# Kernel tuning notes

Measured on AMD Instinct MI355X. Metric: run time of the kernel, lower is better.

The kernel has to match this reference:

```python
import jax, jax.numpy as jnp
import numpy as np

N, E, D, H, ED = 50000, 800000, 128, 8, 64
C = D // H  # head dim = 16


def _ln(x, g, b, eps=1e-5):
    m = jnp.mean(x, axis=-1, keepdims=True)
    v = jnp.var(x, axis=-1, keepdims=True)
    return (x - m) * jax.lax.rsqrt(v + eps) * g + b


def setup_inputs() -> dict:
    key = jax.random.key(0)
    ks = jax.random.split(key, 16)
    p = lambda k, shape: (jax.random.normal(k, shape, dtype=jnp.float32) * 0.05)
    return {
        "x": jax.random.normal(ks[0], (N, D), dtype=jnp.float32),
        "edge_index": jax.random.randint(ks[1], (2, E), 0, N, dtype=jnp.int64),
        "edge_attr": jax.random.normal(ks[2], (E, ED), dtype=jnp.float32),
        "Wq": p(ks[3], (D, D)), "bq": jnp.zeros((D,), jnp.float32),
        "Wk": p(ks[4], (D, D)), "bk": jnp.zeros((D,), jnp.float32),
        "Wv": p(ks[5], (D, D)), "bv": jnp.zeros((D,), jnp.float32),
        "We": p(ks[6], (ED, D)),  # lin_edge has no bias in PyG TransformerConv
        "Wskip": p(ks[7], (D, D)), "bskip": jnp.zeros((D,), jnp.float32),
        "g1": jnp.ones((D,), jnp.float32), "b1": jnp.zeros((D,), jnp.float32),
        "g2": jnp.ones((D,), jnp.float32), "b2": jnp.zeros((D,), jnp.float32),
        "Wf1": p(ks[8], (D, 4 * D)), "bf1": jnp.zeros((4 * D,), jnp.float32),
        "Wf2": p(ks[9], (4 * D, D)), "bf2": jnp.zeros((D,), jnp.float32),
    }


def reference(x, edge_index, edge_attr, Wq, bq, Wk, bk, Wv, bv, We,
              Wskip, bskip, g1, b1, g2, b2, Wf1, bf1, Wf2, bf2):
    n = x.shape[0]
    src, dst = edge_index[0], edge_index[1]  # message flows src (j) -> dst (i)
    q = (x @ Wq + bq).reshape(n, H, C)
    k = (x @ Wk + bk).reshape(n, H, C)
    v = (x @ Wv + bv).reshape(n, H, C)
    e = (edge_attr @ We).reshape(-1, H, C)
    k_j = k[src] + e            # [E,H,C]
    v_j = v[src] + e            # [E,H,C]
    logits = jnp.sum(q[dst] * k_j, axis=-1) / np.sqrt(C)  # [E,H]
    # segment softmax over edges grouped by destination node
    m = jax.ops.segment_max(logits, dst, num_segments=n)   # [N,H]
    ex = jnp.exp(logits - m[dst])
    denom = jax.ops.segment_sum(ex, dst, num_segments=n)   # [N,H]
    alpha = ex / denom[dst]                                 # [E,H]
    agg = jax.ops.segment_sum(alpha[..., None] * v_j, dst, num_segments=n)
    conv = agg.reshape(n, D) + x @ Wskip + bskip            # root_weight skip
    h = _ln(conv + x, g1, b1)
    ffn = jax.nn.gelu(h @ Wf1 + bf1, approximate=False) @ Wf2 + bf2
    return _ln(ffn + h, g2, b2)
```

## Files before the change

### kernel.cpp

```cpp
#include <hip/hip_runtime.h>

#define NN 50000
#define NE 800000

__global__ __launch_bounds__(256) void init_int_kernel(int* __restrict__ a, int n) {
  int i = blockIdx.x * 256 + threadIdx.x;
  if (i < n) a[i] = 0;
}

__global__ __launch_bounds__(256) void hist_kernel(const int* __restrict__ ei,
                                                   int* __restrict__ deg) {
  int e = blockIdx.x * 256 + threadIdx.x;
  if (e < NE) {
    int d = ei[NE + e];
    if ((unsigned)d >= NN) d = 0;
    atomicAdd(&deg[d], 1);
  }
}

__global__ __launch_bounds__(1024) void scan_kernel(const int* __restrict__ deg,
                                                    int* __restrict__ offs) {
  __shared__ int part[1024];
  int tid = threadIdx.x;
  const int chunk = (NN + 1023) / 1024;
  int base = tid * chunk;
  int s = 0;
  for (int j = 0; j < chunk; ++j) {
    int idx = base + j;
    if (idx < NN) s += deg[idx];
  }
  part[tid] = s;
  __syncthreads();
  for (int off = 1; off < 1024; off <<= 1) {
    int t = (tid >= off) ? part[tid - off] : 0;
    __syncthreads();
    part[tid] += t;
    __syncthreads();
  }
  int run = (tid > 0) ? part[tid - 1] : 0;
  for (int j = 0; j < chunk; ++j) {
    int idx = base + j;
    if (idx < NN) { offs[idx] = run; run += deg[idx]; }
  }
  if (tid == 1023) offs[NN] = part[1023];
}

__global__ __launch_bounds__(256) void scatter_kernel(const int* __restrict__ ei,
    const int* __restrict__ offs, int* __restrict__ cursor,
    int* __restrict__ csr_eid, int* __restrict__ csr_src) {
  int e = blockIdx.x * 256 + threadIdx.x;
  if (e < NE) {
    int s = ei[e];
    int d = ei[NE + e];
    if ((unsigned)s >= NN) s = 0;
    if ((unsigned)d >= NN) d = 0;
    int pos = atomicAdd(&cursor[d], 1);
    int slot = offs[d] + pos;
    csr_eid[slot] = e;
    csr_src[slot] = s;
  }
}

__global__ __launch_bounds__(256) void node_proj_kernel(
    const float* __restrict__ x,
    const float* __restrict__ Wq, const float* __restrict__ bq,
    const float* __restrict__ Wk, const float* __restrict__ bk,
    const float* __restrict__ Wv, const float* __restrict__ bv,
    const float* __restrict__ Wsk, const float* __restrict__ bsk,
    float* __restrict__ qo, float* __restrict__ ko, float* __restrict__ vo,
    float* __restrict__ so) {
  __shared__ float xs[64 * 128];
  int tid = threadIdx.x;
  int row0 = blockIdx.x * 64;
  int nrows = NN - row0; if (nrows > 64) nrows = 64;
  const float4* xg = (const float4*)(x + (size_t)row0 * 128);
  float4* xs4 = (float4*)xs;
  int nv = nrows * 32;
  for (int i = tid; i < 64 * 32; i += 256)
    if (i < nv) xs4[i] = xg[i];
  __syncthreads();

  int colg = tid & 31;
  int rowg = tid >> 5;
  const float* Wm[4] = {Wq, Wk, Wv, Wsk};
  const float* bm[4] = {bq, bk, bv, bsk};
  float* om[4] = {qo, ko, vo, so};

  for (int m = 0; m < 4; ++m) {
    const float* W = Wm[m];
    float acc[8][4];
    #pragma unroll
    for (int r = 0; r < 8; ++r)
      #pragma unroll
      for (int c = 0; c < 4; ++c) acc[r][c] = 0.f;
    for (int k0 = 0; k0 < 128; k0 += 4) {
      float4 w0 = *(const float4*)(W + (size_t)(k0 + 0) * 128 + colg * 4);
      float4 w1 = *(const float4*)(W + (size_t)(k0 + 1) * 128 + colg * 4);
      float4 w2 = *(const float4*)(W + (size_t)(k0 + 2) * 128 + colg * 4);
      float4 w3 = *(const float4*)(W + (size_t)(k0 + 3) * 128 + colg * 4);
      #pragma unroll
      for (int r = 0; r < 8; ++r) {
        float4 xv = *(const float4*)(&xs[(rowg * 8 + r) * 128 + k0]);
        acc[r][0] += xv.x * w0.x + xv.y * w1.x + xv.z * w2.x + xv.w * w3.x;
        acc[r][1] += xv.x * w0.y + xv.y * w1.y + xv.z * w2.y + xv.w * w3.y;
        acc[r][2] += xv.x * w0.z + xv.y * w1.z + xv.z * w2.z + xv.w * w3.z;
        acc[r][3] += xv.x * w0.w + xv.y * w1.w + xv.z * w2.w + xv.w * w3.w;
      }
    }
    float4 bb = *(const float4*)(bm[m] + colg * 4);
    float* outp = om[m];
    #pragma unroll
    for (int r = 0; r < 8; ++r) {
      int lr = rowg * 8 + r;
      if (lr < nrows) {
        float4 res;
        res.x = acc[r][0] + bb.x;
        res.y = acc[r][1] + bb.y;
        res.z = acc[r][2] + bb.z;
        res.w = acc[r][3] + bb.w;
        if (m == 0) { res.x *= 0.25f; res.y *= 0.25f; res.z *= 0.25f; res.w *= 0.25f; }
        if (m == 3) {
          res.x += xs[lr * 128 + colg * 4 + 0];
          res.y += xs[lr * 128 + colg * 4 + 1];
          res.z += xs[lr * 128 + colg * 4 + 2];
          res.w += xs[lr * 128 + colg * 4 + 3];
        }
        *(float4*)(outp + (size_t)(row0 + lr) * 128 + colg * 4) = res;
      }
    }
  }
}

__global__ __launch_bounds__(256) void qe_kernel(const float* __restrict__ q,
                                                 const float* __restrict__ We,
                                                 float* __restrict__ qe) {
  long idx = (long)blockIdx.x * 256 + threadIdx.x;
  int n = (int)(idx >> 9);
  int r = (int)(idx & 511);
  int h = r >> 6, j = r & 63;
  const float* qp = q + (size_t)n * 128 + h * 16;
  const float* wp = We + (size_t)j * 128 + h * 16;
  float s = 0.f;
  #pragma unroll
  for (int c = 0; c < 16; ++c) s += qp[c] * wp[c];
  qe[idx] = s;
}

__global__ __launch_bounds__(256) void agg_ln1_kernel(
    const float* __restrict__ q, const float* __restrict__ kb,
    const float* __restrict__ vb, const float* __restrict__ qe,
    const float* __restrict__ ea, const float* __restrict__ skipx,
    const float* __restrict__ We,
    const int* __restrict__ offs, const int* __restrict__ csr_eid,
    const int* __restrict__ csr_src,
    const float* __restrict__ g1, const float* __restrict__ b1,
    float* __restrict__ hbuf) {
  __shared__ float ea_s[4][8][68];
  __shared__ float wea_s[4][8][68];
  int tid = threadIdx.x;
  int wave = tid >> 6;
  int lane = tid & 63;
  int node = blockIdx.x * 4 + wave;
  float (*eas)[68] = ea_s[wave];
  float (*weas)[68] = wea_s[wave];

  int g = lane >> 3;
  int hh = lane & 7;

  float q_r[16];
  {
    const float* qp = q + (size_t)node * 128 + hh * 16;
    #pragma unroll
    for (int u = 0; u < 4; ++u) {
      float4 t = *(const float4*)(qp + 4 * u);
      q_r[4*u+0] = t.x; q_r[4*u+1] = t.y; q_r[4*u+2] = t.z; q_r[4*u+3] = t.w;
    }
  }
  float qe_r[64];
  {
    const float* qp = qe + (size_t)node * 512 + hh * 64;
    #pragma unroll
    for (int u = 0; u < 16; ++u) {
      float4 t = *(const float4*)(qp + 4 * u);
      qe_r[4*u+0] = t.x; qe_r[4*u+1] = t.y; qe_r[4*u+2] = t.z; qe_r[4*u+3] = t.w;
    }
  }
  float wea_r[8];
  #pragma unroll
  for (int j = 0; j < 8; ++j) wea_r[j] = 0.f;
  float wv0 = 0.f, wv1 = 0.f, pden = 0.f;

  int base = offs[node];
  int deg = offs[node + 1] - base;

  for (int t0 = 0; t0 < deg; t0 += 8) {
    int myi = t0 + g;
    int valid = myi < deg;
    int slot = base + (valid ? myi : 0);
    int eid = csr_eid[slot];
    int src = csr_src[slot];

    const float4* eap = (const float4*)(ea + (size_t)eid * 64);
    float4 a0 = eap[hh * 2];
    float4 a1 = eap[hh * 2 + 1];
    *(float4*)(&eas[g][hh * 8]) = a0;
    *(float4*)(&eas[g][hh * 8 + 4]) = a1;
    asm volatile("s_waitcnt lgkmcnt(0)" ::: "memory");

    const float* kp = kb + (size_t)src * 128 + hh * 16;
    float lg = 0.f;
    #pragma unroll
    for (int u = 0; u < 4; ++u) {
      float4 kv = *(const float4*)(kp + 4 * u);
      lg += q_r[4*u+0]*kv.x + q_r[4*u+1]*kv.y + q_r[4*u+2]*kv.z + q_r[4*u+3]*kv.w;
    }
    #pragma unroll
    for (int u = 0; u < 16; ++u) {
      float4 av = *(const float4*)(&eas[g][4 * u]);
      lg += qe_r[4*u+0]*av.x + qe_r[4*u+1]*av.y + qe_r[4*u+2]*av.z + qe_r[4*u+3]*av.w;
    }
    float w = valid ? __expf(lg) : 0.f;
    pden += w;

    #pragma unroll
    for (int g2 = 0; g2 < 8; ++g2) {
      int   sg  = __shfl(src, g2 * 8, 64);
      float wgh = __shfl(w, g2 * 8 + g, 64);
      float2 vv = *(const float2*)(vb + (size_t)sg * 128 + lane * 2);
      wv0 += wgh * vv.x;
      wv1 += wgh * vv.y;
      float4 e0 = *(const float4*)(&eas[g2][hh * 8]);
      float4 e1 = *(const float4*)(&eas[g2][hh * 8 + 4]);
      wea_r[0] += wgh * e0.x; wea_r[1] += wgh * e0.y;
      wea_r[2] += wgh * e0.z; wea_r[3] += wgh * e0.w;
      wea_r[4] += wgh * e1.x; wea_r[5] += wgh * e1.y;
      wea_r[6] += wgh * e1.z; wea_r[7] += wgh * e1.w;
    }
    asm volatile("s_waitcnt lgkmcnt(0)" ::: "memory");
  }

  float den = pden;
  den += __shfl_xor(den, 8, 64);
  den += __shfl_xor(den, 16, 64);
  den += __shfl_xor(den, 32, 64);
  float denf = __shfl(den, g, 64);

  *(float4*)(&weas[g][hh * 8])     = make_float4(wea_r[0], wea_r[1], wea_r[2], wea_r[3]);
  *(float4*)(&weas[g][hh * 8 + 4]) = make_float4(wea_r[4], wea_r[5], wea_r[6], wea_r[7]);
  asm volatile("s_waitcnt lgkmcnt(0)" ::: "memory");

  float s0 = wv0, s1 = wv1;
  const float* wep = We + lane * 2;
  #pragma unroll
  for (int u = 0; u < 16; ++u) {
    float4 ww = *(const float4*)(&weas[g][4 * u]);
    float2 p0 = *(const float2*)(wep + (size_t)(4 * u + 0) * 128);
    float2 p1 = *(const float2*)(wep + (size_t)(4 * u + 1) * 128);
    float2 p2 = *(const float2*)(wep + (size_t)(4 * u + 2) * 128);
    float2 p3 = *(const float2*)(wep + (size_t)(4 * u + 3) * 128);
    s0 += ww.x * p0.x + ww.y * p1.x + ww.z * p2.x + ww.w * p3.x;
    s1 += ww.x * p0.y + ww.y * p1.y + ww.z * p2.y + ww.w * p3.y;
  }
  float inv = (deg > 0) ? 1.f / denf : 0.f;
  float2 skv = *(const float2*)(skipx + (size_t)node * 128 + lane * 2);
  float c0 = s0 * inv + skv.x;
  float c1 = s1 * inv + skv.y;

  float sum = c0 + c1;
  float sq = c0 * c0 + c1 * c1;
  #pragma unroll
  for (int o = 1; o < 64; o <<= 1) {
    sum += __shfl_xor(sum, o, 64);
    sq  += __shfl_xor(sq, o, 64);
  }
  float mean = sum * (1.f / 128.f);
  float var = sq * (1.f / 128.f) - mean * mean;
  float rstd = rsqrtf(var + 1e-5f);
  float2 gg = *(const float2*)(g1 + lane * 2);
  float2 bb = *(const float2*)(b1 + lane * 2);
  float h0 = (c0 - mean) * rstd * gg.x + bb.x;
  float h1 = (c1 - mean) * rstd * gg.y + bb.y;
  *(float2*)(hbuf + (size_t)node * 128 + lane * 2) = make_float2(h0, h1);
}

__global__ __launch_bounds__(256) void ffn_ln2_kernel(
    const float* __restrict__ hbuf,
    const float* __restrict__ Wf1, const float* __restrict__ bf1,
    const float* __restrict__ Wf2, const float* __restrict__ bf2,
    const float* __restrict__ g2v, const float* __restrict__ b2v,
    float* __restrict__ out) {
  __shared__ float hs[16 * 128];
  __shared__ float ts[16][516];
  int tid = threadIdx.x;
  size_t row0 = (size_t)blockIdx.x * 16;
  const float4* hg = (const float4*)(hbuf + row0 * 128);
  float4* hs4 = (float4*)hs;
  hs4[tid] = hg[tid];
  hs4[tid + 256] = hg[tid + 256];
  __syncthreads();

  {
    int colg = tid & 63;
    int rowq = tid >> 6;
    float acc[4][8];
    #pragma unroll
    for (int r = 0; r < 4; ++r)
      #pragma unroll
      for (int c = 0; c < 8; ++c) acc[r][c] = 0.f;
    for (int k0 = 0; k0 < 128; k0 += 4) {
      float hva[4][4];
      #pragma unroll
      for (int r = 0; r < 4; ++r) {
        float4 t = *(const float4*)(&hs[(rowq * 4 + r) * 128 + k0]);
        hva[r][0] = t.x; hva[r][1] = t.y; hva[r][2] = t.z; hva[r][3] = t.w;
      }
      #pragma unroll
      for (int kd = 0; kd < 4; ++kd) {
        float4 w0 = *(const float4*)(Wf1 + (size_t)(k0 + kd) * 512 + colg * 8);
        float4 w1 = *(const float4*)(Wf1 + (size_t)(k0 + kd) * 512 + colg * 8 + 4);
        #pragma unroll
        for (int r = 0; r < 4; ++r) {
          float hv = hva[r][kd];
          acc[r][0] += hv * w0.x; acc[r][1] += hv * w0.y;
          acc[r][2] += hv * w0.z; acc[r][3] += hv * w0.w;
          acc[r][4] += hv * w1.x; acc[r][5] += hv * w1.y;
          acc[r][6] += hv * w1.z; acc[r][7] += hv * w1.w;
        }
      }
    }
    float4 bb0 = *(const float4*)(bf1 + colg * 8);
    float4 bb1 = *(const float4*)(bf1 + colg * 8 + 4);
    float bba[8] = {bb0.x, bb0.y, bb0.z, bb0.w, bb1.x, bb1.y, bb1.z, bb1.w};
    #pragma unroll
    for (int r = 0; r < 4; ++r) {
      #pragma unroll
      for (int c = 0; c < 8; ++c) {
        float val = acc[r][c] + bba[c];
        val = 0.5f * val * (1.f + erff(val * 0.70710678118654752440f));
        ts[rowq * 4 + r][colg * 8 + c] = val;
      }
    }
  }
  __syncthreads();
  {
    int row = tid >> 4;
    int cg = tid & 15;
    float f[8];
    #pragma unroll
    for (int c = 0; c < 8; ++c) f[c] = 0.f;
    for (int k0 = 0; k0 < 512; k0 += 4) {
      float4 tt = *(const float4*)(&ts[row][k0]);
      float tva[4] = {tt.x, tt.y, tt.z, tt.w};
      #pragma unroll
      for (int kd = 0; kd < 4; ++kd) {
        float4 w0 = *(const float4*)(Wf2 + (size_t)(k0 + kd) * 128 + cg * 8);
        float4 w1 = *(const float4*)(Wf2 + (size_t)(k0 + kd) * 128 + cg * 8 + 4);
        float tv = tva[kd];
        f[0] += tv * w0.x; f[1] += tv * w0.y; f[2] += tv * w0.z; f[3] += tv * w0.w;
        f[4] += tv * w1.x; f[5] += tv * w1.y; f[6] += tv * w1.z; f[7] += tv * w1.w;
      }
    }
    float4 bb0 = *(const float4*)(bf2 + cg * 8);
    float4 bb1 = *(const float4*)(bf2 + cg * 8 + 4);
    float4 h0 = *(const float4*)(&hs[row * 128 + cg * 8]);
    float4 h1 = *(const float4*)(&hs[row * 128 + cg * 8 + 4]);
    f[0] += bb0.x + h0.x; f[1] += bb0.y + h0.y; f[2] += bb0.z + h0.z; f[3] += bb0.w + h0.w;
    f[4] += bb1.x + h1.x; f[5] += bb1.y + h1.y; f[6] += bb1.z + h1.z; f[7] += bb1.w + h1.w;

    float sum = 0.f, sq = 0.f;
    #pragma unroll
    for (int c = 0; c < 8; ++c) { sum += f[c]; sq += f[c] * f[c]; }
    #pragma unroll
    for (int o = 1; o < 16; o <<= 1) {
      sum += __shfl_xor(sum, o, 64);
      sq  += __shfl_xor(sq, o, 64);
    }
    float mean = sum * (1.f / 128.f);
    float var = sq * (1.f / 128.f) - mean * mean;
    float rstd = rsqrtf(var + 1e-5f);
    float4 gg0 = *(const float4*)(g2v + cg * 8);
    float4 gg1 = *(const float4*)(g2v + cg * 8 + 4);
    float4 vb0 = *(const float4*)(b2v + cg * 8);
    float4 vb1 = *(const float4*)(b2v + cg * 8 + 4);
    float4 o0, o1;
    o0.x = (f[0] - mean) * rstd * gg0.x + vb0.x;
    o0.y = (f[1] - mean) * rstd * gg0.y + vb0.y;
    o0.z = (f[2] - mean) * rstd * gg0.z + vb0.z;
    o0.w = (f[3] - mean) * rstd * gg0.w + vb0.w;
    o1.x = (f[4] - mean) * rstd * gg1.x + vb1.x;
    o1.y = (f[5] - mean) * rstd * gg1.y + vb1.y;
    o1.z = (f[6] - mean) * rstd * gg1.z + vb1.z;
    o1.w = (f[7] - mean) * rstd * gg1.w + vb1.w;
    float* op = out + (row0 + row) * 128 + cg * 8;
    *(float4*)op = o0;
    *(float4*)(op + 4) = o1;
  }
}

extern "C" void kernel_launch(void* const* d_in, const int* in_sizes, int n_in,
                              void* d_out, int out_size, void* d_ws, size_t ws_size,
                              hipStream_t stream) {
  const float* x   = (const float*)d_in[0];
  const int* ei    = (const int*)d_in[1];
  const float* ea  = (const float*)d_in[2];
  const float* Wq  = (const float*)d_in[3];  const float* bq  = (const float*)d_in[4];
  const float* Wk  = (const float*)d_in[5];  const float* bk  = (const float*)d_in[6];
  const float* Wv  = (const float*)d_in[7];  const float* bv  = (const float*)d_in[8];
  const float* We  = (const float*)d_in[9];
  const float* Wsk = (const float*)d_in[10]; const float* bsk = (const float*)d_in[11];
  const float* g1  = (const float*)d_in[12]; const float* b1  = (const float*)d_in[13];
  const float* g2  = (const float*)d_in[14]; const float* b2  = (const float*)d_in[15];
  const float* Wf1 = (const float*)d_in[16]; const float* bf1 = (const float*)d_in[17];
  const float* Wf2 = (const float*)d_in[18]; const float* bf2 = (const float*)d_in[19];
  float* outp = (float*)d_out;

  char* w = (char*)d_ws;
  float* qb   = (float*)w; w += (size_t)NN * 128 * 4;
  float* kb   = (float*)w; w += (size_t)NN * 128 * 4;
  float* vb   = (float*)w; w += (size_t)NN * 128 * 4;
  float* sk   = (float*)w; w += (size_t)NN * 128 * 4;
  float* hb   = sk;
  float* qeb  = (float*)w; w += (size_t)NN * 512 * 4;
  int* deg    = (int*)w;   w += (size_t)NN * 4;
  int* cursor = (int*)w;   w += (size_t)NN * 4;
  int* offs   = (int*)w;   w += (size_t)(NN + 1) * 4;
  int* ceid   = (int*)w;   w += (size_t)NE * 4;
  int* csrc   = (int*)w;   w += (size_t)NE * 4;

  init_int_kernel<<<(2 * NN + 255) / 256, 256, 0, stream>>>(deg, 2 * NN);
  hist_kernel<<<NE / 256, 256, 0, stream>>>(ei, deg);
  scan_kernel<<<1, 1024, 0, stream>>>(deg, offs);
  scatter_kernel<<<NE / 256, 256, 0, stream>>>(ei, offs, cursor, ceid, csrc);
  node_proj_kernel<<<(NN + 63) / 64, 256, 0, stream>>>(x, Wq, bq, Wk, bk, Wv, bv, Wsk, bsk,
                                                       qb, kb, vb, sk);
  qe_kernel<<<NN * 2, 256, 0, stream>>>(qb, We, qeb);
  agg_ln1_kernel<<<NN / 4, 256, 0, stream>>>(qb, kb, vb, qeb, ea, sk, We,
                                             offs, ceid, csrc, g1, b1, hb);
  ffn_ln2_kernel<<<NN / 16, 256, 0, stream>>>(hb, Wf1, bf1, Wf2, bf2, g2, b2, outp);
}
```

Baseline: 1.723 ms.

## Split fused FFN into LDS-tiled GEMM kernels with split-K partials and LN2 epilogue

Result: slower. 6.836 ms (+296.9%).

```diff
diff --git a/kernel.cpp b/kernel.cpp
--- a/kernel.cpp
+++ b/kernel.cpp
@@ -283,118 +283,136 @@
   *(float2*)(hbuf + (size_t)node * 128 + lane * 2) = make_float2(h0, h1);
 }
 
-__global__ __launch_bounds__(256) void ffn_ln2_kernel(
-    const float* __restrict__ hbuf,
-    const float* __restrict__ Wf1, const float* __restrict__ bf1,
-    const float* __restrict__ Wf2, const float* __restrict__ bf2,
+__device__ __forceinline__ void tile_gemm_body(
+    float* __restrict__ Wlds, float* __restrict__ hls,
+    const float* __restrict__ A, int lda, int kofs,
+    const float* __restrict__ W, int ldw, int kw0, int c0w,
+    const float* __restrict__ bias,
+    bool do_gelu,
+    float* __restrict__ Out, int ldo, int c0o, int row0) {
+  int tid = threadIdx.x;
+  for (int i = tid; i < 128 * 32; i += 256) {
+    int k = i >> 5, cq = i & 31;
+    float4 w = *(const float4*)(W + (size_t)(kw0 + k) * ldw + c0w + cq * 4);
+    Wlds[(cq * 4 + 0) * 132 + k] = w.x;
+    Wlds[(cq * 4 + 1) * 132 + k] = w.y;
+    Wlds[(cq * 4 + 2) * 132 + k] = w.z;
+    Wlds[(cq * 4 + 3) * 132 + k] = w.w;
+  }
+  int c4 = tid & 31;
+  int rp = tid >> 5;
+  float bj[4];
+  #pragma unroll
+  for (int j = 0; j < 4; ++j) bj[j] = bias ? bias[c4 + 32 * j] : 0.f;
+  __syncthreads();
+
+  int rows_blk = NN - row0; if (rows_blk > 256) rows_blk = 256;
+  int nbat = (rows_blk + 15) >> 4;
+  for (int b = 0; b < nbat; ++b) {
+    int rb0 = row0 + b * 16;
+    for (int i = tid; i < 512; i += 256) {
+      int r = i >> 5, qq = i & 31;
+      int gr = rb0 + r;
+      float4 v = make_float4(0.f, 0.f, 0.f, 0.f);
+      if (gr < NN) v = *(const float4*)(A + (size_t)gr * lda + kofs + qq * 4);
+      *(float4*)(hls + r * 128 + qq * 4) = v;
+    }
+    __syncthreads();
+
+    float acc0[4], acc1[4];
+    #pragma unroll
+    for (int j = 0; j < 4; ++j) { acc0[j] = bj[j]; acc1[j] = bj[j]; }
+    int r0 = rp * 2, r1 = rp * 2 + 1;
+    #pragma unroll
+    for (int k0 = 0; k0 < 128; k0 += 4) {
+      float4 h0 = *(const float4*)(hls + r0 * 128 + k0);
+      float4 h1 = *(const float4*)(hls + r1 * 128 + k0);
+      #pragma unroll
+      for (int j = 0; j < 4; ++j) {
+        float4 wv = *(const float4*)(Wlds + (c4 + 32 * j) * 132 + k0);
+        acc0[j] += h0.x * wv.x + h0.y * wv.y + h0.z * wv.z + h0.w * wv.w;
+        acc1[j] += h1.x * wv.x + h1.y * wv.y + h1.z * wv.z + h1.w * wv.w;
+      }
+    }
+
+    int gr0 = rb0 + r0, gr1 = rb0 + r1;
+    #pragma unroll
+    for (int j = 0; j < 4; ++j) {
+      float v0 = acc0[j], v1 = acc1[j];
+      if (do_gelu) {
+        v0 = 0.5f * v0 * (1.f + erff(v0 * 0.70710678118654752440f));
+        v1 = 0.5f * v1 * (1.f + erff(v1 * 0.70710678118654752440f));
+      }
+      int col = c0o + c4 + 32 * j;
+      if (gr0 < NN) Out[(size_t)gr0 * ldo + col] = v0;
+      if (gr1 < NN) Out[(size_t)gr1 * ldo + col] = v1;
+    }
+    __syncthreads();
+  }
+}
+
+__global__ __launch_bounds__(256) void ffn1_kernel(
+    const float* __restrict__ hbuf, const float* __restrict__ Wf1,
+    const float* __restrict__ bf1, float* __restrict__ t) {
+  __shared__ float Wlds[128 * 132];
+  __shared__ float hls[16 * 128];
+  int ti = blockIdx.y;
+  tile_gemm_body(Wlds, hls,
+                 hbuf, 128, 0,
+                 Wf1, 512, 0, ti * 128,
+                 bf1 + ti * 128, true,
+                 t, 512, ti * 128, blockIdx.x * 256);
+}
+
+__global__ __launch_bounds__(256) void ffn2a_kernel(
+    const float* __restrict__ t, const float* __restrict__ Wf2,
+    float* __restrict__ p0, float* __restrict__ p1,
+    float* __restrict__ p2, float* __restrict__ p3) {
+  __shared__ float Wlds[128 * 132];
+  __shared__ float hls[16 * 128];
+  int kt = blockIdx.y;
+  float* P = (kt == 0) ? p0 : (kt == 1) ? p1 : (kt == 2) ? p2 : p3;
+  tile_gemm_body(Wlds, hls,
+                 t, 512, kt * 128,
+                 Wf2, 128, kt * 128, 0,
+                 nullptr, false,
+                 P, 128, 0, blockIdx.x * 256);
+}
+
+__global__ __launch_bounds__(256) void ffn2b_kernel(
+    const float* __restrict__ p0, const float* __restrict__ p1,
+    const float* __restrict__ p2, const float* __restrict__ hbuf,
+    const float* __restrict__ bf2,
     const float* __restrict__ g2v, const float* __restrict__ b2v,
     float* __restrict__ out) {
-  __shared__ float hs[16 * 128];
-  __shared__ float ts[16][516];
   int tid = threadIdx.x;
-  size_t row0 = (size_t)blockIdx.x * 16;
-  const float4* hg = (const float4*)(hbuf + row0 * 128);
-  float4* hs4 = (float4*)hs;
-  hs4[tid] = hg[tid];
-  hs4[tid + 256] = hg[tid + 256];
-  __syncthreads();
-
-  {
-    int colg = tid & 63;
-    int rowq = tid >> 6;
-    float acc[4][8];
-    #pragma unroll
-    for (int r = 0; r < 4; ++r)
-      #pragma unroll
-      for (int c = 0; c < 8; ++c) acc[r][c] = 0.f;
-    for (int k0 = 0; k0 < 128; k0 += 4) {
-      float hva[4][4];
-      #pragma unroll
-      for (int r = 0; r < 4; ++r) {
-        float4 t = *(const float4*)(&hs[(rowq * 4 + r) * 128 + k0]);
-        hva[r][0] = t.x; hva[r][1] = t.y; hva[r][2] = t.z; hva[r][3] = t.w;
-      }
-      #pragma unroll
-      for (int kd = 0; kd < 4; ++kd) {
-        float4 w0 = *(const float4*)(Wf1 + (size_t)(k0 + kd) * 512 + colg * 8);
-        float4 w1 = *(const float4*)(Wf1 + (size_t)(k0 + kd) * 512 + colg * 8 + 4);
-        #pragma unroll
-        for (int r = 0; r < 4; ++r) {
-          float hv = hva[r][kd];
-          acc[r][0] += hv * w0.x; acc[r][1] += hv * w0.y;
-          acc[r][2] += hv * w0.z; acc[r][3] += hv * w0.w;
-          acc[r][4] += hv * w1.x; acc[r][5] += hv * w1.y;
-          acc[r][6] += hv * w1.z; acc[r][7] += hv * w1.w;
-        }
-      }
-    }
-    float4 bb0 = *(const float4*)(bf1 + colg * 8);
-    float4 bb1 = *(const float4*)(bf1 + colg * 8 + 4);
-    float bba[8] = {bb0.x, bb0.y, bb0.z, bb0.w, bb1.x, bb1.y, bb1.z, bb1.w};
-    #pragma unroll
-    for (int r = 0; r < 4; ++r) {
-      #pragma unroll
-      for (int c = 0; c < 8; ++c) {
-        float val = acc[r][c] + bba[c];
-        val = 0.5f * val * (1.f + erff(val * 0.70710678118654752440f));
-        ts[rowq * 4 + r][colg * 8 + c] = val;
-      }
-    }
-  }
-  __syncthreads();
-  {
-    int row = tid >> 4;
-    int cg = tid & 15;
-    float f[8];
-    #pragma unroll
-    for (int c = 0; c < 8; ++c) f[c] = 0.f;
-    for (int k0 = 0; k0 < 512; k0 += 4) {
-      float4 tt = *(const float4*)(&ts[row][k0]);
-      float tva[4] = {tt.x, tt.y, tt.z, tt.w};
-      #pragma unroll
-      for (int kd = 0; kd < 4; ++kd) {
-        float4 w0 = *(const float4*)(Wf2 + (size_t)(k0 + kd) * 128 + cg * 8);
-        float4 w1 = *(const float4*)(Wf2 + (size_t)(k0 + kd) * 128 + cg * 8 + 4);
-        float tv = tva[kd];
-        f[0] += tv * w0.x; f[1] += tv * w0.y; f[2] += tv * w0.z; f[3] += tv * w0.w;
-        f[4] += tv * w1.x; f[5] += tv * w1.y; f[6] += tv * w1.z; f[7] += tv * w1.w;
-      }
-    }
-    float4 bb0 = *(const float4*)(bf2 + cg * 8);
-    float4 bb1 = *(const float4*)(bf2 + cg * 8 + 4);
-    float4 h0 = *(const float4*)(&hs[row * 128 + cg * 8]);
-    float4 h1 = *(const float4*)(&hs[row * 128 + cg * 8 + 4]);
-    f[0] += bb0.x + h0.x; f[1] += bb0.y + h0.y; f[2] += bb0.z + h0.z; f[3] += bb0.w + h0.w;
-    f[4] += bb1.x + h1.x; f[5] += bb1.y + h1.y; f[6] += bb1.z + h1.z; f[7] += bb1.w + h1.w;
-
-    float sum = 0.f, sq = 0.f;
-    #pragma unroll
-    for (int c = 0; c < 8; ++c) { sum += f[c]; sq += f[c] * f[c]; }
-    #pragma unroll
-    for (int o = 1; o < 16; o <<= 1) {
-      sum += __shfl_xor(sum, o, 64);
-      sq  += __shfl_xor(sq, o, 64);
-    }
-    float mean = sum * (1.f / 128.f);
-    float var = sq * (1.f / 128.f) - mean * mean;
-    float rstd = rsqrtf(var + 1e-5f);
-    float4 gg0 = *(const float4*)(g2v + cg * 8);
-    float4 gg1 = *(const float4*)(g2v + cg * 8 + 4);
-    float4 vb0 = *(const float4*)(b2v + cg * 8);
-    float4 vb1 = *(const float4*)(b2v + cg * 8 + 4);
-    float4 o0, o1;
-    o0.x = (f[0] - mean) * rstd * gg0.x + vb0.x;
-    o0.y = (f[1] - mean) * rstd * gg0.y + vb0.y;
-    o0.z = (f[2] - mean) * rstd * gg0.z + vb0.z;
-    o0.w = (f[3] - mean) * rstd * gg0.w + vb0.w;
-    o1.x = (f[4] - mean) * rstd * gg1.x + vb1.x;
-    o1.y = (f[5] - mean) * rstd * gg1.y + vb1.y;
-    o1.z = (f[6] - mean) * rstd * gg1.z + vb1.z;
-    o1.w = (f[7] - mean) * rstd * gg1.w + vb1.w;
-    float* op = out + (row0 + row) * 128 + cg * 8;
-    *(float4*)op = o0;
-    *(float4*)(op + 4) = o1;
-  }
+  int lane = tid & 63;
+  int node = blockIdx.x * 4 + (tid >> 6);
+  size_t base = (size_t)node * 128 + lane * 2;
+  float2 a0 = *(const float2*)(p0 + base);
+  float2 a1 = *(const float2*)(p1 + base);
+  float2 a2 = *(const float2*)(p2 + base);
+  float2 a3 = *(const float2*)(out + base);
+  float2 hh = *(const float2*)(hbuf + base);
+  float2 bb = *(const float2*)(bf2 + lane * 2);
+  float c0 = a0.x + a1.x + a2.x + a3.x + bb.x + hh.x;
+  float c1 = a0.y + a1.y + a2.y + a3.y + bb.y + hh.y;
+
+  float sum = c0 + c1;
+  float sq = c0 * c0 + c1 * c1;
+  #pragma unroll
+  for (int o = 1; o < 64; o <<= 1) {
+    sum += __shfl_xor(sum, o, 64);
+    sq  += __shfl_xor(sq, o, 64);
+  }
+  float mean = sum * (1.f / 128.f);
+  float var = sq * (1.f / 128.f) - mean * mean;
+  float rstd = rsqrtf(var + 1e-5f);
+  float2 gg = *(const float2*)(g2v + lane * 2);
+  float2 b2 = *(const float2*)(b2v + lane * 2);
+  float o0 = (c0 - mean) * rstd * gg.x + b2.x;
+  float o1 = (c1 - mean) * rstd * gg.y + b2.y;
+  *(float2*)(out + base) = make_float2(o0, o1);
 }
 
 extern "C" void kernel_launch(void* const* d_in, const int* in_sizes, int n_in,
@@ -436,5 +454,8 @@
   qe_kernel<<<NN * 2, 256, 0, stream>>>(qb, We, qeb);
   agg_ln1_kernel<<<NN / 4, 256, 0, stream>>>(qb, kb, vb, qeb, ea, sk, We,
                                              offs, ceid, csrc, g1, b1, hb);
-  ffn_ln2_kernel<<<NN / 16, 256, 0, stream>>>(hb, Wf1, bf1, Wf2, bf2, g2, b2, outp);
-}
+  dim3 g196x4(196, 4);
+  ffn1_kernel<<<g196x4, 256, 0, stream>>>(hb, Wf1, bf1, qeb);
+  ffn2a_kernel<<<g196x4, 256, 0, stream>>>(qeb, Wf2, qb, kb, vb, outp);
+  ffn2b_kernel<<<NN / 4, 256, 0, stream>>>(qb, kb, vb, hb, bf2, g2, b2, outp);
+}
```
